# Optimization experiments

Hardware: AMD Instinct MI355X
Metric: run time of the kernel (lower is better)

The kernel has to match this reference:

```python
import jax, jax.numpy as jnp
import numpy as np

# Dimensions matching init_kwargs
O = 4096   # out_features
I = 4096   # in_features
R = 32     # svd_rank
G = 64     # n_groups
GS = I // G  # group_size = 64
NBITS = 4
NUM_BYTES = O * I * NBITS // 8


def setup_inputs() -> dict:
    key = jax.random.key(0)
    ks = jax.random.split(key, 7)
    return {
        "x": jax.random.normal(ks[0], (1, 4096, I), dtype=jnp.float32),
        # bit-packed int4 weights, two nibbles per byte (stored as int32 holding 0..255)
        "w_packed": jax.random.randint(ks[1], (NUM_BYTES,), 0, 256, dtype=jnp.int32),
        "svd_up": jax.random.normal(ks[2], (O, R), dtype=jnp.float32) * 0.02,
        "svd_down": jax.random.normal(ks[3], (R, I), dtype=jnp.float32) * 0.02,
        "scale": jax.random.uniform(ks[4], (O, G, 1), dtype=jnp.float32, minval=0.001, maxval=0.02),
        "zero_point": jax.random.uniform(ks[5], (O, G, 1), dtype=jnp.float32, minval=0.0, maxval=15.0),
        "bias": jax.random.normal(ks[6], (O,), dtype=jnp.float32) * 0.01,
    }


def _dequantize(w_packed, svd_up, svd_down, scale, zero_point):
    # Unpack two 4-bit values per byte (low nibble first).
    low = w_packed & 0xF
    high = (w_packed >> 4) & 0xF
    w_q = jnp.stack([low, high], axis=-1).reshape(O, G, GS).astype(jnp.float32)
    # Per-group affine dequant: (q - zero) * scale, then SVD low-rank correction.
    W = ((w_q - zero_point) * scale).reshape(O, I)
    return W + svd_up @ svd_down  # [O, I]


def reference(x, w_packed, svd_up, svd_down, scale, zero_point, bias):
    # forward_int8 path (tokens > 16, int8_matmul=True)
    W_f = _dequantize(w_packed, svd_up, svd_down, scale, zero_point).T  # [I, O]
    xm = x.reshape(-1, I)  # [N, I]
    # Dynamic per-row activation quant
    scale_x = jnp.max(jnp.abs(xm), axis=1, keepdims=True) / 127.0  # [N, 1]
    x_q = jnp.clip(jnp.round(xm / scale_x), -128, 127).astype(jnp.int8)
    # Dynamic per-column weight quant
    scale_w = jnp.max(jnp.abs(W_f), axis=0, keepdims=True) / 127.0  # [1, O]
    W_q = jnp.clip(jnp.round(W_f / scale_w), -128, 127).astype(jnp.int8)
    # int8 GEMM with int32 accumulation, then dequant scales + bias
    acc = jnp.matmul(x_q.astype(jnp.int32), W_q.astype(jnp.int32))  # [N, O] int32
    out = acc.astype(jnp.float32) * scale_x * scale_w + bias
    return out.reshape(*x.shape[:-1], O)
```

## Files before the change

### kernel.cpp

```cpp
#include <hip/hip_runtime.h>
#include <cstdint>
#include <cstddef>

#define I_DIM 4096
#define O_DIM 4096
#define RNK 32
#define NGRP 64
#define N_TOK 4096

typedef int v4i  __attribute__((ext_vector_type(4)));
typedef int v16i __attribute__((ext_vector_type(16)));

__device__ __forceinline__ int clamp_i8(float v) {
    int q = (int)rintf(v);
    q = q < -128 ? -128 : q;
    q = q > 127 ? 127 : q;
    return q;
}

#define BO 4

__global__ __launch_bounds__(256, 4) void quant_fused_kernel(
    const float* __restrict__ x, char* __restrict__ x_q,
    float* __restrict__ scale_x,
    const int* __restrict__ w_packed, const float* __restrict__ svd_up,
    const float* __restrict__ svd_down, const float* __restrict__ scale,
    const float* __restrict__ zp, char* __restrict__ w_q,
    float* __restrict__ scale_w)
{
    const int tid = threadIdx.x;

    if (blockIdx.x < N_TOK) {
        const int n = blockIdx.x;
        const float4* xr = (const float4*)(x + (size_t)n * I_DIM);
        float4 v[4];
        float m = 0.0f;
#pragma unroll
        for (int j = 0; j < 4; j++) {
            v[j] = xr[tid + 256 * j];
            m = fmaxf(m, fmaxf(fmaxf(fabsf(v[j].x), fabsf(v[j].y)),
                               fmaxf(fabsf(v[j].z), fabsf(v[j].w))));
        }
        __shared__ float sx_red[4];
        __shared__ float s_sx;
        for (int off = 32; off > 0; off >>= 1)
            m = fmaxf(m, __shfl_down(m, off, 64));
        if ((tid & 63) == 0) sx_red[tid >> 6] = m;
        __syncthreads();
        if (tid == 0) {
            const float mm = fmaxf(fmaxf(sx_red[0], sx_red[1]),
                                   fmaxf(sx_red[2], sx_red[3]));
            const float sx = mm / 127.0f;
            scale_x[n] = sx;
            s_sx = sx;
        }
        __syncthreads();
        const float sx = s_sx;
        int* outw = (int*)(x_q + (size_t)n * I_DIM);
#pragma unroll
        for (int j = 0; j < 4; j++) {
            const int q0 = clamp_i8(v[j].x / sx);
            const int q1 = clamp_i8(v[j].y / sx);
            const int q2 = clamp_i8(v[j].z / sx);
            const int q3 = clamp_i8(v[j].w / sx);
            outw[tid + 256 * j] =
                (q0 & 0xFF) | ((q1 & 0xFF) << 8) | ((q2 & 0xFF) << 16) | ((q3 & 0xFF) << 24);
        }
        return;
    }

    const int o0 = (blockIdx.x - N_TOK) * BO;

    __shared__ float s_sc[BO][NGRP];
    __shared__ float s_zp[BO][NGRP];
    __shared__ float s_red[BO][4];
    __shared__ float s_sw[BO];

    for (int t = tid; t < BO * NGRP; t += 256) {
        s_sc[t >> 6][t & 63] = scale[(size_t)(o0 + (t >> 6)) * NGRP + (t & 63)];
        s_zp[t >> 6][t & 63] = zp[(size_t)(o0 + (t >> 6)) * NGRP + (t & 63)];
    }
    __syncthreads();

    float W[4][BO][4];
    float vmax[BO];
#pragma unroll
    for (int ro = 0; ro < BO; ro++) vmax[ro] = 0.0f;

#pragma unroll
    for (int jq = 0; jq < 4; jq++) {
        const int q = tid + 256 * jq;
        const int i = 4 * q;
        const int g = q >> 4;

#pragma unroll
        for (int ro = 0; ro < BO; ro++) {
            const int2 b2 = *(const int2*)&w_packed[(size_t)(o0 + ro) * (I_DIM / 2) + 2 * q];
            const float sc = s_sc[ro][g], z = s_zp[ro][g];
            W[jq][ro][0] = ((float)(b2.x & 0xF) - z) * sc;
            W[jq][ro][1] = ((float)((b2.x >> 4) & 0xF) - z) * sc;
            W[jq][ro][2] = ((float)(b2.y & 0xF) - z) * sc;
            W[jq][ro][3] = ((float)((b2.y >> 4) & 0xF) - z) * sc;
        }

#pragma unroll 4
        for (int r = 0; r < RNK; r++) {
            const float4 d = *(const float4*)&svd_down[(size_t)r * I_DIM + i];
#pragma unroll
            for (int ro = 0; ro < BO; ro++) {
                const float u = svd_up[(size_t)(o0 + ro) * RNK + r];
                W[jq][ro][0] += u * d.x;
                W[jq][ro][1] += u * d.y;
                W[jq][ro][2] += u * d.z;
                W[jq][ro][3] += u * d.w;
            }
        }

#pragma unroll
        for (int ro = 0; ro < BO; ro++) {
            vmax[ro] = fmaxf(vmax[ro],
                fmaxf(fmaxf(fabsf(W[jq][ro][0]), fabsf(W[jq][ro][1])),
                      fmaxf(fabsf(W[jq][ro][2]), fabsf(W[jq][ro][3]))));
        }
    }

    const int lane = tid & 63, wv = tid >> 6;
#pragma unroll
    for (int ro = 0; ro < BO; ro++) {
        float m = vmax[ro];
        for (int off = 32; off > 0; off >>= 1)
            m = fmaxf(m, __shfl_down(m, off, 64));
        if (lane == 0) s_red[ro][wv] = m;
    }
    __syncthreads();
    if (tid < BO) {
        const float m = fmaxf(fmaxf(s_red[tid][0], s_red[tid][1]),
                              fmaxf(s_red[tid][2], s_red[tid][3]));
        const float sw = m / 127.0f;
        scale_w[o0 + tid] = sw;
        s_sw[tid] = sw;
    }
    __syncthreads();

    float inv[BO];
#pragma unroll
    for (int ro = 0; ro < BO; ro++) inv[ro] = 1.0f / s_sw[ro];

#pragma unroll
    for (int jq = 0; jq < 4; jq++) {
        const int q = tid + 256 * jq;
#pragma unroll
        for (int ro = 0; ro < BO; ro++) {
            const int q0 = clamp_i8(W[jq][ro][0] * inv[ro]);
            const int q1 = clamp_i8(W[jq][ro][1] * inv[ro]);
            const int q2 = clamp_i8(W[jq][ro][2] * inv[ro]);
            const int q3 = clamp_i8(W[jq][ro][3] * inv[ro]);
            ((int*)w_q)[(size_t)(o0 + ro) * (I_DIM / 4) + q] =
                (q0 & 0xFF) | ((q1 & 0xFF) << 8) | ((q2 & 0xFF) << 16) | ((q3 & 0xFF) << 24);
        }
    }
}

#define BM 128
#define BN 128
#define BK 128

__global__ __launch_bounds__(256) void gemm_i8_kernel(
    const char* __restrict__ x_q, const char* __restrict__ w_q,
    const float* __restrict__ scale_x, const float* __restrict__ scale_w,
    const float* __restrict__ bias, float* __restrict__ out)
{
    __shared__ v4i As4[BM * BK / 16];
    __shared__ v4i Bs4[BN * BK / 16];
    char* As = (char*)As4;
    char* Bs = (char*)Bs4;

    const int tid = threadIdx.x;
    const int bm0 = blockIdx.x * BM;
    const int bn0 = blockIdx.y * BN;
    const int lane = tid & 63, wv = tid >> 6;
    const int wm = wv & 1, wn = wv >> 1;
    const int l31 = lane & 31, h = lane >> 5;

    v16i acc[2][2];
#pragma unroll
    for (int mt = 0; mt < 2; mt++)
#pragma unroll
        for (int nt = 0; nt < 2; nt++)
            acc[mt][nt] = (v16i)(0);

    for (int kk = 0; kk < I_DIM / BK; kk++) {
        const int k0 = kk * BK;
#pragma unroll
        for (int j = 0; j < 4; j++) {
            const int c = tid + 256 * j;
            const int row = c >> 3;
            const int kc = (c & 7) ^ (row & 7);
            const char* ga = x_q + (size_t)(bm0 + row) * I_DIM + k0 + kc * 16;
            __builtin_amdgcn_global_load_lds(
                (const __attribute__((address_space(1))) unsigned int*)ga,
                (__attribute__((address_space(3))) unsigned int*)(As + c * 16),
                16, 0, 0);
            const char* gb = w_q + (size_t)(bn0 + row) * I_DIM + k0 + kc * 16;
            __builtin_amdgcn_global_load_lds(
                (const __attribute__((address_space(1))) unsigned int*)gb,
                (__attribute__((address_space(3))) unsigned int*)(Bs + c * 16),
                16, 0, 0);
        }
        __syncthreads();
#pragma unroll
        for (int s = 0; s < 4; s++) {
            v4i af[2], bf[2];
#pragma unroll
            for (int mt = 0; mt < 2; mt++) {
                const int row = wm * 64 + mt * 32 + l31;
                const int kc = (s * 2 + h) ^ (row & 7);
                af[mt] = *(const v4i*)(As + row * BK + kc * 16);
            }
#pragma unroll
            for (int nt = 0; nt < 2; nt++) {
                const int row = wn * 64 + nt * 32 + l31;
                const int kc = (s * 2 + h) ^ (row & 7);
                bf[nt] = *(const v4i*)(Bs + row * BK + kc * 16);
            }
#pragma unroll
            for (int mt = 0; mt < 2; mt++)
#pragma unroll
                for (int nt = 0; nt < 2; nt++)
                    acc[mt][nt] = __builtin_amdgcn_mfma_i32_32x32x32_i8(
                        af[mt], bf[nt], acc[mt][nt], 0, 0, 0);
        }
        __syncthreads();
    }

#pragma unroll
    for (int mt = 0; mt < 2; mt++) {
        const int rbase = bm0 + wm * 64 + mt * 32 + 4 * h;
        float sx[16];
#pragma unroll
        for (int reg = 0; reg < 16; reg++)
            sx[reg] = scale_x[rbase + (reg & 3) + 8 * (reg >> 2)];
#pragma unroll
        for (int nt = 0; nt < 2; nt++) {
            const int oc = bn0 + wn * 64 + nt * 32 + l31;
            const float sw = scale_w[oc];
            const float bs = bias[oc];
#pragma unroll
            for (int reg = 0; reg < 16; reg++) {
                const int rr = rbase + (reg & 3) + 8 * (reg >> 2);
                out[(size_t)rr * O_DIM + oc] =
                    (float)acc[mt][nt][reg] * sx[reg] * sw + bs;
            }
        }
    }
}

extern "C" void kernel_launch(void* const* d_in, const int* in_sizes, int n_in,
                              void* d_out, int out_size, void* d_ws, size_t ws_size,
                              hipStream_t stream) {
    const float* x        = (const float*)d_in[0];
    const int*   w_packed = (const int*)d_in[1];
    const float* svd_up   = (const float*)d_in[2];
    const float* svd_down = (const float*)d_in[3];
    const float* scale    = (const float*)d_in[4];
    const float* zp       = (const float*)d_in[5];
    const float* bias     = (const float*)d_in[6];
    float* out = (float*)d_out;

    char* ws = (char*)d_ws;
    char*  w_q     = ws;
    char*  x_q     = ws + ((size_t)16 << 20);
    float* scale_w = (float*)(ws + ((size_t)32 << 20));
    float* scale_x = (float*)(ws + ((size_t)32 << 20) + 16384);

    quant_fused_kernel<<<N_TOK + O_DIM / BO, 256, 0, stream>>>(
        x, x_q, scale_x, w_packed, svd_up, svd_down, scale, zp, w_q, scale_w);
    gemm_i8_kernel<<<dim3(N_TOK / BM, O_DIM / BN), 256, 0, stream>>>(
        x_q, w_q, scale_x, scale_w, bias, out);
}
```

Baseline: 256.3 us.

## Split fused quant kernel and remap GEMM blocks for XCD-local L2 reuse

Splits the fused activation/weight quantization kernel into two separate kernels, so each gets its own launch bounds and register budget instead of sharing the heavier weight-path footprint. It also remaps GEMM block IDs so that blocks landing on the same XCD (id mod 8) share a group of four N-tiles and sweep all M-tiles, aiming to improve L2 hit rates for weight tiles. The cost is an extra kernel launch, and the remap assumes the 32x32 tile grid and round-robin dispatch across 8 XCDs.

```diff
diff --git a/kernel.cpp b/kernel.cpp
--- a/kernel.cpp
+++ b/kernel.cpp
@@ -20,61 +20,19 @@
 
 #define BO 4
 
-__global__ __launch_bounds__(256, 4) void quant_fused_kernel(
-    const float* __restrict__ x, char* __restrict__ x_q,
-    float* __restrict__ scale_x,
+__global__ __launch_bounds__(256, 4) void quant_w_kernel(
     const int* __restrict__ w_packed, const float* __restrict__ svd_up,
     const float* __restrict__ svd_down, const float* __restrict__ scale,
     const float* __restrict__ zp, char* __restrict__ w_q,
     float* __restrict__ scale_w)
 {
-    const int tid = threadIdx.x;
-
-    if (blockIdx.x < N_TOK) {
-        const int n = blockIdx.x;
-        const float4* xr = (const float4*)(x + (size_t)n * I_DIM);
-        float4 v[4];
-        float m = 0.0f;
-#pragma unroll
-        for (int j = 0; j < 4; j++) {
-            v[j] = xr[tid + 256 * j];
-            m = fmaxf(m, fmaxf(fmaxf(fabsf(v[j].x), fabsf(v[j].y)),
-                               fmaxf(fabsf(v[j].z), fabsf(v[j].w))));
-        }
-        __shared__ float sx_red[4];
-        __shared__ float s_sx;
-        for (int off = 32; off > 0; off >>= 1)
-            m = fmaxf(m, __shfl_down(m, off, 64));
-        if ((tid & 63) == 0) sx_red[tid >> 6] = m;
-        __syncthreads();
-        if (tid == 0) {
-            const float mm = fmaxf(fmaxf(sx_red[0], sx_red[1]),
-                                   fmaxf(sx_red[2], sx_red[3]));
-            const float sx = mm / 127.0f;
-            scale_x[n] = sx;
-            s_sx = sx;
-        }
-        __syncthreads();
-        const float sx = s_sx;
-        int* outw = (int*)(x_q + (size_t)n * I_DIM);
-#pragma unroll
-        for (int j = 0; j < 4; j++) {
-            const int q0 = clamp_i8(v[j].x / sx);
-            const int q1 = clamp_i8(v[j].y / sx);
-            const int q2 = clamp_i8(v[j].z / sx);
-            const int q3 = clamp_i8(v[j].w / sx);
-            outw[tid + 256 * j] =
-                (q0 & 0xFF) | ((q1 & 0xFF) << 8) | ((q2 & 0xFF) << 16) | ((q3 & 0xFF) << 24);
-        }
-        return;
-    }
-
-    const int o0 = (blockIdx.x - N_TOK) * BO;
-
     __shared__ float s_sc[BO][NGRP];
     __shared__ float s_zp[BO][NGRP];
     __shared__ float s_red[BO][4];
     __shared__ float s_sw[BO];
+
+    const int tid = threadIdx.x;
+    const int o0 = blockIdx.x * BO;
 
     for (int t = tid; t < BO * NGRP; t += 256) {
         s_sc[t >> 6][t & 63] = scale[(size_t)(o0 + (t >> 6)) * NGRP + (t & 63)];
@@ -158,6 +116,48 @@
             ((int*)w_q)[(size_t)(o0 + ro) * (I_DIM / 4) + q] =
                 (q0 & 0xFF) | ((q1 & 0xFF) << 8) | ((q2 & 0xFF) << 16) | ((q3 & 0xFF) << 24);
         }
+    }
+}
+
+__global__ __launch_bounds__(256) void quant_x_kernel(
+    const float* __restrict__ x, char* __restrict__ x_q,
+    float* __restrict__ scale_x)
+{
+    const int n = blockIdx.x;
+    const int tid = threadIdx.x;
+    const float4* xr = (const float4*)(x + (size_t)n * I_DIM);
+    float4 v[4];
+    float m = 0.0f;
+#pragma unroll
+    for (int j = 0; j < 4; j++) {
+        v[j] = xr[tid + 256 * j];
+        m = fmaxf(m, fmaxf(fmaxf(fabsf(v[j].x), fabsf(v[j].y)),
+                           fmaxf(fabsf(v[j].z), fabsf(v[j].w))));
+    }
+    __shared__ float s_red[4];
+    __shared__ float s_sx;
+    for (int off = 32; off > 0; off >>= 1)
+        m = fmaxf(m, __shfl_down(m, off, 64));
+    if ((tid & 63) == 0) s_red[tid >> 6] = m;
+    __syncthreads();
+    if (tid == 0) {
+        const float mm = fmaxf(fmaxf(s_red[0], s_red[1]),
+                               fmaxf(s_red[2], s_red[3]));
+        const float sx = mm / 127.0f;
+        scale_x[n] = sx;
+        s_sx = sx;
+    }
+    __syncthreads();
+    const float sx = s_sx;
+    int* outw = (int*)(x_q + (size_t)n * I_DIM);
+#pragma unroll
+    for (int j = 0; j < 4; j++) {
+        const int q0 = clamp_i8(v[j].x / sx);
+        const int q1 = clamp_i8(v[j].y / sx);
+        const int q2 = clamp_i8(v[j].z / sx);
+        const int q3 = clamp_i8(v[j].w / sx);
+        outw[tid + 256 * j] =
+            (q0 & 0xFF) | ((q1 & 0xFF) << 8) | ((q2 & 0xFF) << 16) | ((q3 & 0xFF) << 24);
     }
 }
 
@@ -176,8 +176,12 @@
     char* Bs = (char*)Bs4;
 
     const int tid = threadIdx.x;
-    const int bm0 = blockIdx.x * BM;
-    const int bn0 = blockIdx.y * BN;
+    const int id = blockIdx.x;
+    const int xcd = id & 7;
+    const int s_lin = id >> 3;
+    const int bm0 = (s_lin & 31) * BM;
+    const int bn0 = (xcd * 4 + (s_lin >> 5)) * BN;
+
     const int lane = tid & 63, wv = tid >> 6;
     const int wm = wv & 1, wn = wv >> 1;
     const int l31 = lane & 31, h = lane >> 5;
@@ -273,8 +277,9 @@
     float* scale_w = (float*)(ws + ((size_t)32 << 20));
     float* scale_x = (float*)(ws + ((size_t)32 << 20) + 16384);
 
-    quant_fused_kernel<<<N_TOK + O_DIM / BO, 256, 0, stream>>>(
-        x, x_q, scale_x, w_packed, svd_up, svd_down, scale, zp, w_q, scale_w);
-    gemm_i8_kernel<<<dim3(N_TOK / BM, O_DIM / BN), 256, 0, stream>>>(
+    quant_w_kernel<<<O_DIM / BO, 256, 0, stream>>>(w_packed, svd_up, svd_down,
+                                                   scale, zp, w_q, scale_w);
+    quant_x_kernel<<<N_TOK, 256, 0, stream>>>(x, x_q, scale_x);
+    gemm_i8_kernel<<<(N_TOK / BM) * (O_DIM / BN), 256, 0, stream>>>(
         x_q, w_q, scale_x, scale_w, bias, out);
 }
```

New measurement: 254.5 us. About the same (-0.7%).
